# Kernel optimization log

Measured on AMD Instinct MI355X. Metric: run time of the kernel, lower is better.

## Reference

```python
import jax, jax.numpy as jnp
import numpy as np

N_NODES = 100000
N_EDGES = 1600000
IN_DIM, HID_DIM, OUT_DIM = 128, 256, 128


def gcn_conv(x, src, dst, W, b, n):
    # PyG GCNConv: linear transform, add self-loops, symmetric normalization,
    # scatter-sum aggregation over destination nodes, then bias.
    h = x @ W  # [n, d_out]
    loops = jnp.arange(n, dtype=src.dtype)
    s = jnp.concatenate([src, loops])
    d = jnp.concatenate([dst, loops])
    deg = jax.ops.segment_sum(jnp.ones_like(d, dtype=h.dtype), d, num_segments=n)
    dinv = jnp.where(deg > 0, jax.lax.rsqrt(deg), 0.0)
    norm = dinv[s] * dinv[d]  # [E+n]
    msg = h[s] * norm[:, None]  # gather + scale
    out = jax.ops.segment_sum(msg, d, num_segments=n)  # scatter-reduce
    return out + b


def layer_norm(x, gamma, beta, eps=1e-5):
    mu = jnp.mean(x, axis=-1, keepdims=True)
    var = jnp.mean(jnp.square(x - mu), axis=-1, keepdims=True)
    return (x - mu) * jax.lax.rsqrt(var + eps) * gamma + beta


def setup_inputs() -> dict:
    key = jax.random.key(0)
    ks = jax.random.split(key, 8)
    x = jax.random.normal(ks[0], (N_NODES, IN_DIM), dtype=jnp.float32)
    edge_index = jax.random.randint(ks[1], (2, N_EDGES), 0, N_NODES, dtype=jnp.int64)
    W1 = jax.random.normal(ks[2], (IN_DIM, HID_DIM), dtype=jnp.float32) * (1.0 / np.sqrt(IN_DIM))
    b1 = jnp.zeros((HID_DIM,), dtype=jnp.float32)
    W2 = jax.random.normal(ks[3], (HID_DIM, OUT_DIM), dtype=jnp.float32) * (1.0 / np.sqrt(HID_DIM))
    b2 = jnp.zeros((OUT_DIM,), dtype=jnp.float32)
    gamma = jnp.ones((OUT_DIM,), dtype=jnp.float32)
    beta = jnp.zeros((OUT_DIM,), dtype=jnp.float32)
    return {"x": x, "edge_index": edge_index, "W1": W1, "b1": b1,
            "W2": W2, "b2": b2, "gamma": gamma, "beta": beta}


def reference(x, edge_index, W1, b1, W2, b2, gamma, beta):
    n = x.shape[0]
    src, dst = edge_index[0], edge_index[1]
    h = gcn_conv(x, src, dst, W1, b1, n)
    h = jax.nn.relu(h)
    # dropout(p=0.1) is identity in eval mode
    h = gcn_conv(h, src, dst, W2, b2, n)
    return layer_norm(h, gamma, beta)
```

## Files before the change

kernel.cpp:

```cpp
#include <hip/hip_runtime.h>
#include <hip/hip_fp16.h>
#include <stdint.h>

#define N_NODES 100000
#define N_EDGES 1600000
#define IN_DIM  128
#define HID_DIM 256
#define OUT_DIM 128
#define RS 264
#define NBUCK 391
#define EPB   2048
#define PADB  5120
#define PB    782
#define WB    256

typedef __attribute__((ext_vector_type(8))) _Float16 f16x8;
typedef __attribute__((ext_vector_type(4))) float f32x4;

__device__ __forceinline__ int clampi(int v) {
    v = v < 0 ? 0 : v;
    return v >= N_NODES ? N_NODES - 1 : v;
}
__device__ __forceinline__ float2 h2f2(uint32_t u) {
    union { uint32_t u; __half2 h; } c; c.u = u;
    return __half22float2(c.h);
}
__device__ __forceinline__ uint32_t packh(float a, float b) {
    union { __half2 h; uint32_t u; } c; c.h = __floats2half2_rn(a, b);
    return c.u;
}
__device__ __forceinline__ uint16_t f2h(float a) {
    union { __half h; uint16_t s; } c; c.h = __float2half_rn(a);
    return c.s;
}

__device__ __forceinline__ int src_at(const int* ei, int isI64, int e) {
    return clampi(isI64 ? ei[2 * (size_t)e] : ei[e]);
}
__device__ __forceinline__ int dst_at(const int* ei, int isI64, int e) {
    return clampi(isI64 ? ei[2 * (size_t)N_EDGES + 2 * (size_t)e]
                        : ei[(size_t)N_EDGES + e]);
}


__global__ __launch_bounds__(256) void partition_kernel(const int* __restrict__ ei,
                                                        int* __restrict__ cursor,
                                                        uint32_t* __restrict__ recs,
                                                        const float* __restrict__ W1,
                                                        uint16_t* __restrict__ W1t,
                                                        const float* __restrict__ W2,
                                                        uint16_t* __restrict__ W2t) {
    if (blockIdx.x >= PB) {
        int idx = (blockIdx.x - PB) * 256 + threadIdx.x;
        if (idx < IN_DIM * HID_DIM) {
            int k = idx / HID_DIM, n = idx - k * HID_DIM;
            W1t[n * IN_DIM + k] = f2h(W1[idx]);
        } else {
            int j = idx - IN_DIM * HID_DIM;
            int k = j / OUT_DIM, n = j - k * OUT_DIM;
            W2t[n * HID_DIM + k] = f2h(W2[j]);
        }
        return;
    }
    __shared__ int hist[NBUCK];
    __shared__ int histBase[NBUCK];
    __shared__ int gBase[NBUCK];
    __shared__ int scanT[512];
    __shared__ uint32_t lrec[EPB];
    __shared__ int s_flag;
    int tid = threadIdx.x;
    if (tid == 0) {
        int z = 1;
        #pragma unroll
        for (int i = 0; i < 16; ++i)
            if (ei[2 * i + 1] != 0) z = 0;
        s_flag = z;
    }
    for (int b = tid; b < NBUCK; b += 256) hist[b] = 0;
    __syncthreads();
    int isI64 = s_flag;
    int base = blockIdx.x * EPB;
    int srcs[8], dsts[8], slots[8];
    #pragma unroll
    for (int r = 0; r < 8; ++r) {
        int e = base + r * 256 + tid;
        slots[r] = -1;
        srcs[r] = 0; dsts[r] = 0;
        if (e < N_EDGES) {
            srcs[r] = src_at(ei, isI64, e);
            dsts[r] = dst_at(ei, isI64, e);
            slots[r] = atomicAdd(&hist[dsts[r] >> 8], 1);
        }
    }
    __syncthreads();
    scanT[tid]       = (tid < NBUCK) ? hist[tid] : 0;
    scanT[tid + 256] = (tid + 256 < NBUCK) ? hist[tid + 256] : 0;
    __syncthreads();
    for (int off = 1; off < 512; off <<= 1) {
        int v0 = (tid >= off) ? scanT[tid - off] : 0;
        int v1 = scanT[tid + 256 - off];
        __syncthreads();
        if (tid >= off) scanT[tid] += v0;
        scanT[tid + 256] += v1;
        __syncthreads();
    }
    for (int b = tid; b < NBUCK; b += 256) {
        histBase[b] = b ? scanT[b - 1] : 0;
        if (hist[b] > 0) gBase[b] = atomicAdd(&cursor[b], hist[b]);
    }
    __syncthreads();
    #pragma unroll
    for (int r = 0; r < 8; ++r) {
        if (slots[r] >= 0) {
            int b = dsts[r] >> 8;
            lrec[histBase[b] + slots[r]] =
                ((uint32_t)srcs[r] << 8) | (uint32_t)(dsts[r] & 255);
        }
    }
    __syncthreads();
    int nvalid = N_EDGES - base; if (nvalid > EPB) nvalid = EPB;
    for (int i = tid; i < nvalid; i += 256) {
        uint32_t rec = lrec[i];
        int lo = 0, hi = NBUCK - 1;
        while (lo < hi) {
            int mid = (lo + hi) >> 1;
            if (scanT[mid] > i) hi = mid; else lo = mid + 1;
        }
        int b = lo;
        int pos = gBase[b] + (i - histBase[b]);
        if (pos < PADB)
            recs[(size_t)b * PADB + pos] = rec;
    }
}


__global__ __launch_bounds__(256) void build_kernel(const uint32_t* __restrict__ recs,
                                                    const int* __restrict__ cursor,
                                                    int* __restrict__ row_ptr,
                                                    float* __restrict__ dinv,
                                                    int* __restrict__ colv,
                                                    const float* __restrict__ x,
                                                    uint2* __restrict__ xsout) {
    __shared__ uint32_t lrec[PADB];
    __shared__ int cnt[256];
    __shared__ int lofs[256];
    __shared__ int cur[256];
    __shared__ int scanT[256];
    int b = blockIdx.x, tid = threadIdx.x;
    int nb = cursor[b]; if (nb > PADB) nb = PADB;
    int pv = 0;
    for (int j = tid; j < b; j += 256) {
        int c = cursor[j];
        pv += (c > PADB) ? PADB : c;
    }
    cnt[tid] = 0; cur[tid] = 0;
    scanT[tid] = pv;
    __syncthreads();
    for (int off = 128; off > 0; off >>= 1) {
        if (tid < off) scanT[tid] += scanT[tid + off];
        __syncthreads();
    }
    int cbase = scanT[0];
    __syncthreads();
    for (int i = tid; i < nb; i += 256) {
        uint32_t r = recs[(size_t)b * PADB + i];
        lrec[i] = r;
        atomicAdd(&cnt[r & 255], 1);
    }
    __syncthreads();
    scanT[tid] = cnt[tid];
    __syncthreads();
    for (int off = 1; off < 256; off <<= 1) {
        int x2 = (tid >= off) ? scanT[tid - off] : 0;
        __syncthreads();
        if (tid >= off) scanT[tid] += x2;
        __syncthreads();
    }
    lofs[tid] = tid ? scanT[tid - 1] : 0;
    int node = b * 256 + tid;
    if (node < N_NODES) {
        row_ptr[node] = cbase + lofs[tid];
        dinv[node] = rsqrtf((float)(cnt[tid] + 1));
    }
    if (b == NBUCK - 1 && tid == 0) row_ptr[N_NODES] = cbase + nb;
    __syncthreads();
    for (int i = tid; i < nb; i += 256) {
        uint32_t r = lrec[i];
        int id = (int)(r & 255);
        int slot = atomicAdd(&cur[id], 1);
        colv[cbase + lofs[id] + slot] = (int)(r >> 8);
    }
    const float4* x4 = (const float4*)x + (size_t)b * 8192;
    uint2* xo = xsout + (size_t)b * 8192;
    int lim = (N_NODES - b * 256) * 32; if (lim > 8192) lim = 8192;
    for (int j = tid; j < lim; j += 256) {
        float d = rsqrtf((float)(cnt[j >> 5] + 1));
        float4 v = x4[j];
        uint2 o;
        o.x = packh(d * v.x, d * v.y);
        o.y = packh(d * v.z, d * v.w);
        xo[j] = o;
    }
}


template<bool LN>
__global__ __launch_bounds__(256) void agg_kernel(const uint4* __restrict__ rows,
                                                  const int* __restrict__ row_ptr,
                                                  const int* __restrict__ colv,
                                                  const float* __restrict__ dinv,
                                                  const float* __restrict__ bias,
                                                  const float* __restrict__ gamma,
                                                  const float* __restrict__ beta,
                                                  float* __restrict__ out,
                                                  uint4* __restrict__ out16) {
    int node = blockIdx.x * 16 + (threadIdx.x >> 4);
    if (node >= N_NODES) return;
    int l = threadIdx.x & 15;
    const char* base = (const char*)rows + ((unsigned)l << 4);
    float di = dinv[node];
    float acc[8];
    {
        uint4 u = *(const uint4*)(base + ((unsigned)node << 8));
        float2 f0 = h2f2(u.x), f1 = h2f2(u.y), f2 = h2f2(u.z), f3 = h2f2(u.w);
        acc[0] = f0.x; acc[1] = f0.y; acc[2] = f1.x; acc[3] = f1.y;
        acc[4] = f2.x; acc[5] = f2.y; acc[6] = f3.x; acc[7] = f3.y;
    }
    int e = row_ptr[node], e1 = row_ptr[node + 1];
    int s0 = 0, s1 = 0, s2 = 0, s3 = 0;
    if (e     < e1) s0 = colv[e];
    if (e + 1 < e1) s1 = colv[e + 1];
    if (e + 2 < e1) s2 = colv[e + 2];
    if (e + 3 < e1) s3 = colv[e + 3];
    while (e + 4 <= e1) {
        uint4 v0 = *(const uint4*)(base + ((unsigned)s0 << 8));
        uint4 v1 = *(const uint4*)(base + ((unsigned)s1 << 8));
        uint4 v2 = *(const uint4*)(base + ((unsigned)s2 << 8));
        uint4 v3 = *(const uint4*)(base + ((unsigned)s3 << 8));
        int p0 = (e + 4 < e1) ? e + 4 : e;
        int p1 = (e + 5 < e1) ? e + 5 : e;
        int p2 = (e + 6 < e1) ? e + 6 : e;
        int p3 = (e + 7 < e1) ? e + 7 : e;
        int t0 = colv[p0], t1 = colv[p1], t2 = colv[p2], t3 = colv[p3];
        {
            float2 f0 = h2f2(v0.x), f1 = h2f2(v0.y), f2 = h2f2(v0.z), f3 = h2f2(v0.w);
            acc[0] += f0.x; acc[1] += f0.y; acc[2] += f1.x; acc[3] += f1.y;
            acc[4] += f2.x; acc[5] += f2.y; acc[6] += f3.x; acc[7] += f3.y;
        }
        {
            float2 f0 = h2f2(v1.x), f1 = h2f2(v1.y), f2 = h2f2(v1.z), f3 = h2f2(v1.w);
            acc[0] += f0.x; acc[1] += f0.y; acc[2] += f1.x; acc[3] += f1.y;
            acc[4] += f2.x; acc[5] += f2.y; acc[6] += f3.x; acc[7] += f3.y;
        }
        {
            float2 f0 = h2f2(v2.x), f1 = h2f2(v2.y), f2 = h2f2(v2.z), f3 = h2f2(v2.w);
            acc[0] += f0.x; acc[1] += f0.y; acc[2] += f1.x; acc[3] += f1.y;
            acc[4] += f2.x; acc[5] += f2.y; acc[6] += f3.x; acc[7] += f3.y;
        }
        {
            float2 f0 = h2f2(v3.x), f1 = h2f2(v3.y), f2 = h2f2(v3.z), f3 = h2f2(v3.w);
            acc[0] += f0.x; acc[1] += f0.y; acc[2] += f1.x; acc[3] += f1.y;
            acc[4] += f2.x; acc[5] += f2.y; acc[6] += f3.x; acc[7] += f3.y;
        }
        s0 = t0; s1 = t1; s2 = t2; s3 = t3; e += 4;
    }
    int r = e1 - e;
    if (r > 0) {
        uint4 v = *(const uint4*)(base + ((unsigned)s0 << 8));
        float2 f0 = h2f2(v.x), f1 = h2f2(v.y), f2 = h2f2(v.z), f3 = h2f2(v.w);
        acc[0] += f0.x; acc[1] += f0.y; acc[2] += f1.x; acc[3] += f1.y;
        acc[4] += f2.x; acc[5] += f2.y; acc[6] += f3.x; acc[7] += f3.y;
    }
    if (r > 1) {
        uint4 v = *(const uint4*)(base + ((unsigned)s1 << 8));
        float2 f0 = h2f2(v.x), f1 = h2f2(v.y), f2 = h2f2(v.z), f3 = h2f2(v.w);
        acc[0] += f0.x; acc[1] += f0.y; acc[2] += f1.x; acc[3] += f1.y;
        acc[4] += f2.x; acc[5] += f2.y; acc[6] += f3.x; acc[7] += f3.y;
    }
    if (r > 2) {
        uint4 v = *(const uint4*)(base + ((unsigned)s2 << 8));
        float2 f0 = h2f2(v.x), f1 = h2f2(v.y), f2 = h2f2(v.z), f3 = h2f2(v.w);
        acc[0] += f0.x; acc[1] += f0.y; acc[2] += f1.x; acc[3] += f1.y;
        acc[4] += f2.x; acc[5] += f2.y; acc[6] += f3.x; acc[7] += f3.y;
    }
    if (!LN) {
        uint4 o;
        o.x = packh(acc[0] * di, acc[1] * di);
        o.y = packh(acc[2] * di, acc[3] * di);
        o.z = packh(acc[4] * di, acc[5] * di);
        o.w = packh(acc[6] * di, acc[7] * di);
        out16[(size_t)node * 16 + l] = o;
    } else {
        const float4* b4 = (const float4*)(bias + l * 8);
        float4 bb0 = b4[0], bb1 = b4[1];
        float v[8];
        v[0] = acc[0] * di + bb0.x; v[1] = acc[1] * di + bb0.y;
        v[2] = acc[2] * di + bb0.z; v[3] = acc[3] * di + bb0.w;
        v[4] = acc[4] * di + bb1.x; v[5] = acc[5] * di + bb1.y;
        v[6] = acc[6] * di + bb1.z; v[7] = acc[7] * di + bb1.w;
        float s = 0.f;
        #pragma unroll
        for (int j = 0; j < 8; ++j) s += v[j];
        #pragma unroll
        for (int o = 8; o > 0; o >>= 1) s += __shfl_xor(s, o, 64);
        float mu = s * (1.0f / 128.0f);
        float q = 0.f;
        #pragma unroll
        for (int j = 0; j < 8; ++j) { v[j] -= mu; q += v[j] * v[j]; }
        #pragma unroll
        for (int o = 8; o > 0; o >>= 1) q += __shfl_xor(q, o, 64);
        float rstd = rsqrtf(q * (1.0f / 128.0f) + 1e-5f);
        const float4* g4 = (const float4*)(gamma + l * 8);
        const float4* t4 = (const float4*)(beta + l * 8);
        float4 g0 = g4[0], g1 = g4[1], t0 = t4[0], t1 = t4[1];
        float* orow = out + (size_t)node * 128 + l * 8;
        f32x4 o0, o1;
        o0.x = v[0] * rstd * g0.x + t0.x; o0.y = v[1] * rstd * g0.y + t0.y;
        o0.z = v[2] * rstd * g0.z + t0.z; o0.w = v[3] * rstd * g0.w + t0.w;
        o1.x = v[4] * rstd * g1.x + t1.x; o1.y = v[5] * rstd * g1.y + t1.y;
        o1.z = v[6] * rstd * g1.z + t1.z; o1.w = v[7] * rstd * g1.w + t1.w;
        __builtin_nontemporal_store(o0, (f32x4*)orow);
        __builtin_nontemporal_store(o1, (f32x4*)(orow + 4));
    }
}


__global__ __launch_bounds__(256) void fused_gemm_kernel(const uint16_t* __restrict__ A16,
                                                         const uint16_t* __restrict__ W1t,
                                                         const float* __restrict__ b1,
                                                         const uint16_t* __restrict__ W2t,
                                                         const float* __restrict__ dinv,
                                                         uint16_t* __restrict__ G16, int M) {
    __shared__ __align__(16) uint16_t Hs[64 * RS];
    int lane = threadIdx.x & 63;
    int wave = threadIdx.x >> 6;
    int r15 = lane & 15;
    int quad = lane >> 4;
    int kofs = quad * 8;
    int blk_row = blockIdx.x * 64;

    f16x8 a[4][4];
    #pragma unroll
    for (int mt = 0; mt < 4; ++mt) {
        bool valid = (blk_row + mt * 16) < M;
        int row = valid ? (blk_row + mt * 16 + r15) : 0;
        const uint16_t* arow = A16 + (size_t)row * IN_DIM + kofs;
        #pragma unroll
        for (int ks = 0; ks < 4; ++ks)
            a[mt][ks] = *(const f16x8*)(arow + ks * 32);
    }

    #pragma unroll
    for (int nt = 0; nt < 4; ++nt) {
        int ncol = (wave * 4 + nt) * 16 + r15;
        const uint16_t* bp = W1t + (size_t)ncol * IN_DIM + kofs;
        f32x4 acc[4];
        #pragma unroll
        for (int mt = 0; mt < 4; ++mt) acc[mt] = (f32x4){0.f, 0.f, 0.f, 0.f};
        #pragma unroll
        for (int ks = 0; ks < 4; ++ks) {
            f16x8 bv = *(const f16x8*)(bp + ks * 32);
            #pragma unroll
            for (int mt = 0; mt < 4; ++mt)
                acc[mt] = __builtin_amdgcn_mfma_f32_16x16x32_f16(a[mt][ks], bv, acc[mt], 0, 0, 0);
        }
        float bb = b1[ncol];
        #pragma unroll
        for (int mt = 0; mt < 4; ++mt) {
            #pragma unroll
            for (int r = 0; r < 4; ++r) {
                int lrow = mt * 16 + quad * 4 + r;
                Hs[lrow * RS + ncol] = f2h(fmaxf(acc[mt][r] + bb, 0.f));
            }
        }
    }
    __syncthreads();

    #pragma unroll
    for (int nt = 0; nt < 2; ++nt) {
        int ncol = (wave * 2 + nt) * 16 + r15;
        const uint16_t* bp = W2t + (size_t)ncol * HID_DIM + kofs;
        f16x8 b2[8];
        #pragma unroll
        for (int ks = 0; ks < 8; ++ks)
            b2[ks] = *(const f16x8*)(bp + ks * 32);
        f32x4 acc[4];
        #pragma unroll
        for (int mt = 0; mt < 4; ++mt) acc[mt] = (f32x4){0.f, 0.f, 0.f, 0.f};
        #pragma unroll
        for (int ks = 0; ks < 8; ++ks) {
            #pragma unroll
            for (int mt = 0; mt < 4; ++mt) {
                f16x8 av = *(const f16x8*)(Hs + (mt * 16 + r15) * RS + ks * 32 + kofs);
                acc[mt] = __builtin_amdgcn_mfma_f32_16x16x32_f16(av, b2[ks], acc[mt], 0, 0, 0);
            }
        }
        #pragma unroll
        for (int mt = 0; mt < 4; ++mt) {
            if ((blk_row + mt * 16) < M) {
                #pragma unroll
                for (int r = 0; r < 4; ++r) {
                    int row = blk_row + mt * 16 + quad * 4 + r;
                    G16[(size_t)row * OUT_DIM + ncol] = f2h(dinv[row] * acc[mt][r]);
                }
            }
        }
    }
}


extern "C" void kernel_launch(void* const* d_in, const int* in_sizes, int n_in,
                              void* d_out, int out_size, void* d_ws, size_t ws_size,
                              hipStream_t stream) {
    const float* x     = (const float*)d_in[0];
    const int*   ei    = (const int*)d_in[1];
    const float* W1    = (const float*)d_in[2];
    const float* b1    = (const float*)d_in[3];
    const float* W2    = (const float*)d_in[4];
    const float* b2    = (const float*)d_in[5];
    const float* gamma = (const float*)d_in[6];
    const float* beta  = (const float*)d_in[7];

    char* ws = (char*)d_ws;
    size_t off = 0;
    auto alloc = [&](size_t bytes) -> void* {
        void* p = ws + off;
        off += (bytes + 511) & ~(size_t)511;
        return p;
    };
    int*      cursor  = (int*)alloc((size_t)NBUCK * 4);
    int*      row_ptr = (int*)alloc((size_t)(N_NODES + 1) * 4);
    float*    dinv    = (float*)alloc((size_t)N_NODES * 4);
    uint16_t* W1t     = (uint16_t*)alloc((size_t)IN_DIM * HID_DIM * 2);
    uint16_t* W2t     = (uint16_t*)alloc((size_t)HID_DIM * OUT_DIM * 2);
    int*      colv    = (int*)alloc((size_t)N_EDGES * 4);
    void*     big     = alloc((size_t)N_NODES * IN_DIM * 2);
    uint32_t* recs    = (uint32_t*)big;
    uint16_t* g16     = (uint16_t*)big;
    if (ws_size < off) return;

    uint2*    xs16 = (uint2*)d_out;
    uint16_t* xa16 = (uint16_t*)d_out + (size_t)N_NODES * IN_DIM;

    const int AB = (N_NODES + 15) / 16;
    const int GB = (N_NODES + 63) / 64;

    hipMemsetAsync(cursor, 0, (size_t)NBUCK * 4, stream);
    partition_kernel<<<PB + WB, 256, 0, stream>>>(ei, cursor, recs, W1, W1t, W2, W2t);
    build_kernel<<<NBUCK, 256, 0, stream>>>(recs, cursor, row_ptr, dinv, colv, x, xs16);
    agg_kernel<false><<<AB, 256, 0, stream>>>((const uint4*)xs16, row_ptr, colv, dinv,
                                              nullptr, nullptr, nullptr,
                                              nullptr, (uint4*)xa16);
    fused_gemm_kernel<<<GB, 256, 0, stream>>>(xa16, W1t, b1, W2t, dinv, g16, N_NODES);
    agg_kernel<true><<<AB, 256, 0, stream>>>((const uint4*)g16, row_ptr, colv, dinv,
                                             b2, gamma, beta, (float*)d_out, nullptr);
}
```

Measured before the change: 340.4 us.

## Scatter edge records directly to buckets, dropping LDS staging and scan

The bucketing kernel no longer stages records in shared memory, runs a prefix scan and binary-searches to write them out coalesced. Each thread now writes its record straight to the global bucket slot given by the atomic slot plus the block's bucket base. Edges per block double so there are half as many blocks and fewer global cursor atomics. This cuts synchronisation and shared-memory work but turns the global stores into scattered writes, and the 16-deep register arrays raise register pressure.

```diff
diff --git a/kernel.cpp b/kernel.cpp
--- a/kernel.cpp
+++ b/kernel.cpp
@@ -9,9 +9,9 @@
 #define OUT_DIM 128
 #define RS 264
 #define NBUCK 391
-#define EPB   2048
+#define EPB   4096
 #define PADB  5120
-#define PB    782
+#define PB    391
 #define WB    256
 
 typedef __attribute__((ext_vector_type(8))) _Float16 f16x8;
@@ -63,10 +63,7 @@
         return;
     }
     __shared__ int hist[NBUCK];
-    __shared__ int histBase[NBUCK];
     __shared__ int gBase[NBUCK];
-    __shared__ int scanT[512];
-    __shared__ uint32_t lrec[EPB];
     __shared__ int s_flag;
     int tid = threadIdx.x;
     if (tid == 0) {
@@ -80,9 +77,9 @@
     __syncthreads();
     int isI64 = s_flag;
     int base = blockIdx.x * EPB;
-    int srcs[8], dsts[8], slots[8];
+    int srcs[16], dsts[16], slots[16];
     #pragma unroll
-    for (int r = 0; r < 8; ++r) {
+    for (int r = 0; r < 16; ++r) {
         int e = base + r * 256 + tid;
         slots[r] = -1;
         srcs[r] = 0; dsts[r] = 0;
@@ -93,43 +90,18 @@
         }
     }
     __syncthreads();
-    scanT[tid]       = (tid < NBUCK) ? hist[tid] : 0;
-    scanT[tid + 256] = (tid + 256 < NBUCK) ? hist[tid + 256] : 0;
-    __syncthreads();
-    for (int off = 1; off < 512; off <<= 1) {
-        int v0 = (tid >= off) ? scanT[tid - off] : 0;
-        int v1 = scanT[tid + 256 - off];
-        __syncthreads();
-        if (tid >= off) scanT[tid] += v0;
-        scanT[tid + 256] += v1;
-        __syncthreads();
-    }
-    for (int b = tid; b < NBUCK; b += 256) {
-        histBase[b] = b ? scanT[b - 1] : 0;
+    for (int b = tid; b < NBUCK; b += 256)
         if (hist[b] > 0) gBase[b] = atomicAdd(&cursor[b], hist[b]);
-    }
     __syncthreads();
     #pragma unroll
-    for (int r = 0; r < 8; ++r) {
+    for (int r = 0; r < 16; ++r) {
         if (slots[r] >= 0) {
             int b = dsts[r] >> 8;
-            lrec[histBase[b] + slots[r]] =
-                ((uint32_t)srcs[r] << 8) | (uint32_t)(dsts[r] & 255);
-        }
-    }
-    __syncthreads();
-    int nvalid = N_EDGES - base; if (nvalid > EPB) nvalid = EPB;
-    for (int i = tid; i < nvalid; i += 256) {
-        uint32_t rec = lrec[i];
-        int lo = 0, hi = NBUCK - 1;
-        while (lo < hi) {
-            int mid = (lo + hi) >> 1;
-            if (scanT[mid] > i) hi = mid; else lo = mid + 1;
-        }
-        int b = lo;
-        int pos = gBase[b] + (i - histBase[b]);
-        if (pos < PADB)
-            recs[(size_t)b * PADB + pos] = rec;
+            int pos = gBase[b] + slots[r];
+            if (pos < PADB)
+                recs[(size_t)b * PADB + pos] =
+                    ((uint32_t)srcs[r] << 8) | (uint32_t)(dsts[r] & 255);
+        }
     }
 }
 
```

Result: faster. 327.3 us (-3.9%).
